# Kernel optimization log

Measured on AMD Instinct MI355X. Metric: run time of the kernel, lower is better.

Reference implementation:

```python
import jax, jax.numpy as jnp
import numpy as np

B, S, D, H = 2, 2048, 2048, 16
DK = D // H


def setup_inputs() -> dict:
    key = jax.random.key(0)
    k1, k2, k3 = jax.random.split(key, 3)
    x = jax.random.normal(k1, (B, S, D), dtype=jnp.float32)
    # trunc-normal in the original; plain normal with matching std is fine for a numeric baseline
    std_qkv = 2.0 / (DK + D)  # note: original passes variance as std to trunc_normal_
    W_qkv = jax.random.normal(k2, (3 * D, D), dtype=jnp.float32) * std_qkv
    W_o = jax.random.normal(k3, (D, D), dtype=jnp.float32) * (1.0 / D)
    return {"x": x, "W_qkv": W_qkv, "W_o": W_o}


def reference(x, W_qkv, W_o):
    b, s, d = x.shape
    # fused QKV projection: y = x @ W_qkv^T
    qkv = jnp.einsum('bsd,ed->bse', x, W_qkv)  # [b, s, 3d]
    q, k, v = jnp.split(qkv, 3, axis=-1)
    # [b, s, d] -> [b, h, s, dk]
    def to_heads(t):
        return t.reshape(b, s, H, DK).transpose(0, 2, 1, 3)
    q, k, v = to_heads(q), to_heads(k), to_heads(v)
    scores = jnp.einsum('bhqd,bhkd->bhqk', q, k) / np.sqrt(DK).astype(np.float32)
    causal = jnp.tril(jnp.ones((s, s), dtype=bool))
    scores = jnp.where(causal, scores, -jnp.inf)
    att = jax.nn.softmax(scores, axis=-1)
    out = jnp.einsum('bhqk,bhkd->bhqd', att, v)  # [b, h, s, dk]
    out = out.transpose(0, 2, 1, 3).reshape(b, s, d)
    return jnp.einsum('bsd,od->bso', out, W_o)
```

## Files before the change

kernel.cpp:

```cpp
#include <hip/hip_runtime.h>

typedef _Float16 f16;
typedef _Float16 f16x4 __attribute__((ext_vector_type(4)));
typedef _Float16 f16x8 __attribute__((ext_vector_type(8)));
typedef float    f32x4 __attribute__((ext_vector_type(4)));

#define MFMA_F16(a,b,c) __builtin_amdgcn_mfma_f32_16x16x32_f16((a),(b),(c),0,0,0)

static constexpr int B_  = 2;
static constexpr int S_  = 2048;
static constexpr int D_  = 2048;
static constexpr int H_  = 16;
static constexpr int DK_ = 128;
static constexpr int K_  = 2048;

__device__ __forceinline__ void gload_lds16(const void* g, void* l) {
  __builtin_amdgcn_global_load_lds(
      (const __attribute__((address_space(1))) void*)g,
      (__attribute__((address_space(3))) void*)l, 16, 0, 0);
}

__global__ __launch_bounds__(256) void cast_all_kernel(const float* __restrict__ x,
                                                       const float* __restrict__ wqkv,
                                                       const float* __restrict__ wo,
                                                       f16* __restrict__ xb,
                                                       f16* __restrict__ wqkvb,
                                                       f16* __restrict__ wob) {
  const int total = 6291456;
  int i = blockIdx.x * 256 + threadIdx.x;
  int stride = gridDim.x * 256;
  for (int j = i; j < total; j += stride) {
    const float* src; f16* dst; int jj;
    if (j < 2097152)      { src = x;    dst = xb;    jj = j; }
    else if (j < 5242880) { src = wqkv; dst = wqkvb; jj = j - 2097152; }
    else                  { src = wo;   dst = wob;   jj = j - 5242880; }
    float4 v = reinterpret_cast<const float4*>(src)[jj];
    f16x4 o = {(f16)v.x, (f16)v.y, (f16)v.z, (f16)v.w};
    reinterpret_cast<f16x4*>(dst)[jj] = o;
  }
}


#define SYNCW0                                          \
  asm volatile("s_waitcnt vmcnt(0)" ::: "memory");      \
  __builtin_amdgcn_s_barrier();                         \
  asm volatile("" ::: "memory");

__device__ __forceinline__ void stage2(const f16* gA, const f16* gB, char* slot, int w) {
  gload_lds16(gA,      slot +         w * 1024);
  gload_lds16(gA + 32, slot +  8192 + w * 1024);
  gload_lds16(gB,      slot + 16384 + w * 1024);
  gload_lds16(gB + 32, slot + 24576 + w * 1024);
}

__device__ __forceinline__ void compute2(const char* slot, int aoff, int boff, int lro,
                                         f32x4 (&acc)[4][2]) {
  f16x8 a0[4], b0[2], a1[4], b1[2];
#pragma unroll
  for (int mi = 0; mi < 4; ++mi) {
    a0[mi] = *(const f16x8*)(slot +        aoff + mi * 1024 + lro);
    a1[mi] = *(const f16x8*)(slot + 8192 + aoff + mi * 1024 + lro);
  }
#pragma unroll
  for (int ni = 0; ni < 2; ++ni) {
    b0[ni] = *(const f16x8*)(slot + 16384 + boff + ni * 1024 + lro);
    b1[ni] = *(const f16x8*)(slot + 24576 + boff + ni * 1024 + lro);
  }
  __builtin_amdgcn_s_setprio(1);
#pragma unroll
  for (int mi = 0; mi < 4; ++mi)
#pragma unroll
    for (int ni = 0; ni < 2; ++ni)
      acc[mi][ni] = MFMA_F16(a0[mi], b0[ni], acc[mi][ni]);
#pragma unroll
  for (int mi = 0; mi < 4; ++mi)
#pragma unroll
    for (int ni = 0; ni < 2; ++ni)
      acc[mi][ni] = MFMA_F16(a1[mi], b1[ni], acc[mi][ni]);
  __builtin_amdgcn_s_setprio(0);
}

__device__ __forceinline__ void gemm_core_db(const f16* __restrict__ A,
                                             const f16* __restrict__ Bw,
                                             int brow, int bcol, char* lds,
                                             f32x4 (&acc)[4][2]) {
  const int tid = threadIdx.x;
  const int w = tid >> 6, l = tid & 63;
  const int lg = l >> 4, lr = l & 15;
  const int wm = w >> 2, wn = w & 3;
  const int lro = (lr * 4 + (lg ^ ((lr >> 1) & 3))) * 16;
  const int aoff = wm * 4096;
  const int boff = wn * 2048;

#pragma unroll
  for (int mi = 0; mi < 4; ++mi)
#pragma unroll
    for (int ni = 0; ni < 2; ++ni) acc[mi][ni] = (f32x4){0.f, 0.f, 0.f, 0.f};

  const int kgsrc = (l & 3) ^ ((l >> 3) & 3);
  const f16* gA = A  + (size_t)(brow * 128 + w * 16 + (l >> 2)) * K_ + kgsrc * 8;
  const f16* gB = Bw + (size_t)(bcol * 128 + w * 16 + (l >> 2)) * K_ + kgsrc * 8;

  char* s0 = lds;
  char* s1 = lds + 32768;

  stage2(gA, gB, s0, w);
  SYNCW0

  for (int tb = 0; tb < 16; ++tb) {
    const int t = tb * 2;
    stage2(gA + (size_t)(t + 1) * 64, gB + (size_t)(t + 1) * 64, s1, w);
    compute2(s0, aoff, boff, lro, acc);
    SYNCW0
    if (tb < 15)
      stage2(gA + (size_t)(t + 2) * 64, gB + (size_t)(t + 2) * 64, s0, w);
    compute2(s1, aoff, boff, lro, acc);
    SYNCW0
  }
}

__global__ __launch_bounds__(512, 4) void gemm_qkv_kernel(const f16* __restrict__ xb,
                                                          const f16* __restrict__ wqkv,
                                                          f16* __restrict__ Q,
                                                          f16* __restrict__ Kk,
                                                          f16* __restrict__ Vt) {
  __shared__ __align__(16) char lds[65536];
  const int bid = blockIdx.x;
  const int xcd = bid & 7;
  const int local = bid >> 3;
  const int brow = xcd * 4 + (local & 3);
  const int bcol = local >> 2;

  f32x4 acc[4][2];
  gemm_core_db(xb, wqkv, brow, bcol, lds, acc);

  const int tid = threadIdx.x;
  const int w = tid >> 6, l = tid & 63;
  const int lg = l >> 4, lr = l & 15;
  const int wm = w >> 2, wn = w & 3;

  const int which = bcol >> 4;
  const int h = bcol & 15;

  if (which == 2) {
#pragma unroll
    for (int mi = 0; mi < 4; ++mi) {
      const int m0 = brow * 128 + wm * 64 + mi * 16 + lg * 4;
      const int b = m0 >> 11, s = m0 & 2047;
#pragma unroll
      for (int ni = 0; ni < 2; ++ni) {
        const int dk = wn * 32 + ni * 16 + lr;
        f16x4 v = {(f16)acc[mi][ni][0], (f16)acc[mi][ni][1],
                   (f16)acc[mi][ni][2], (f16)acc[mi][ni][3]};
        *(f16x4*)(Vt + ((size_t)(b * H_ + h) * DK_ + dk) * S_ + s) = v;
      }
    }
  } else {
    f16* outp = (which == 0) ? Q : Kk;
    const float scale = (which == 0) ? 0.08838834764831845f : 1.0f;
#pragma unroll
    for (int mi = 0; mi < 4; ++mi) {
      const int m0 = brow * 128 + wm * 64 + mi * 16 + lg * 4;
#pragma unroll
      for (int ni = 0; ni < 2; ++ni) {
        const int dk = wn * 32 + ni * 16 + lr;
#pragma unroll
        for (int r = 0; r < 4; ++r) {
          const int mm = m0 + r;
          const int b = mm >> 11, s = mm & 2047;
          outp[(((size_t)b * H_ + h) * S_ + s) * DK_ + dk] = (f16)(acc[mi][ni][r] * scale);
        }
      }
    }
  }
}

__global__ __launch_bounds__(512, 4) void gemm_out_kernel(const f16* __restrict__ ab,
                                                          const f16* __restrict__ wo,
                                                          float* __restrict__ out) {
  __shared__ __align__(16) char lds[65536];
  const int bid = blockIdx.x;
  const int xcd = bid & 7;
  const int local = bid >> 3;
  const int brow = xcd * 4 + (local & 3);
  const int bcol = local >> 2;

  f32x4 acc[4][2];
  gemm_core_db(ab, wo, brow, bcol, lds, acc);

  const int tid = threadIdx.x;
  const int w = tid >> 6, l = tid & 63;
  const int lg = l >> 4, lr = l & 15;
  const int wm = w >> 2, wn = w & 3;

#pragma unroll
  for (int mi = 0; mi < 4; ++mi) {
    const int m0 = brow * 128 + wm * 64 + mi * 16 + lg * 4;
#pragma unroll
    for (int ni = 0; ni < 2; ++ni) {
      const int n = bcol * 128 + wn * 32 + ni * 16 + lr;
#pragma unroll
      for (int r = 0; r < 4; ++r)
        out[(size_t)(m0 + r) * D_ + n] = acc[mi][ni][r];
    }
  }
}

__global__ __launch_bounds__(256) void attn_kernel(const f16* __restrict__ Q,
                                                   const f16* __restrict__ Kg,
                                                   const f16* __restrict__ Vt,
                                                   f16* __restrict__ O) {
  __shared__ __align__(16) char Kbuf2[2][16384];
  __shared__ __align__(16) char Vbuf2[2][16384];
  __shared__ __align__(16) unsigned char Ps[4][2048];

  const int bid = blockIdx.x;
  const int pr = bid & 15;
  const int h  = (bid >> 4) & 15;
  const int b  = bid >> 8;
  const int bh = b * H_ + h;
  const int tid = threadIdx.x;
  const int w = tid >> 6, l = tid & 63;
  const int lg = l >> 4, lr = l & 15;
  const int lrow = l >> 2;
  const int kgsrc = (l & 3) ^ ((l >> 3) & 3);
  const int lro = (lr * 4 + (lg ^ ((lr >> 1) & 3))) * 16;

  const f16* Kbase = Kg + (size_t)bh * S_ * DK_;
  const f16* Vbase = Vt + (size_t)bh * DK_ * S_;

  for (int half = 0; half < 2; ++half) {
    const int qt = half ? (31 - pr) : pr;

    const f16* Qg = Q + ((size_t)bh * S_ + qt * 64 + w * 16) * DK_;
    f16x8 qf[4];
#pragma unroll
    for (int kd = 0; kd < 4; ++kd)
      qf[kd] = *(const f16x8*)(Qg + (size_t)lr * DK_ + kd * 32 + lg * 8);

    f32x4 o[8];
#pragma unroll
    for (int n = 0; n < 8; ++n) o[n] = (f32x4){0.f, 0.f, 0.f, 0.f};
    float mrun[4] = {-1e30f, -1e30f, -1e30f, -1e30f};
    float lrun[4] = {0.f, 0.f, 0.f, 0.f};

    const int ntiles = qt + 1;

    {
      const f16* Kt = Kbase;
      const f16* Vp = Vbase;
#pragma unroll
      for (int i = 0; i < 4; ++i) {
        const int u = w * 4 + i;
        gload_lds16(Kt + (size_t)((u >> 2) * 16 + lrow) * DK_ + (u & 3) * 32 + kgsrc * 8,
                    Kbuf2[0] + u * 1024);
      }
#pragma unroll
      for (int i = 0; i < 4; ++i) {
        const int u = w * 4 + i;
        gload_lds16(Vp + (size_t)((u >> 1) * 16 + lrow) * S_ + (u & 1) * 32 + kgsrc * 8,
                    Vbuf2[0] + u * 1024);
      }
    }

    for (int kt = 0; kt < ntiles; ++kt) {
      const int cur = kt & 1;
      if (kt + 1 < ntiles) {
        const f16* Kt = Kbase + (size_t)(kt + 1) * 64 * DK_;
        const f16* Vp = Vbase + (kt + 1) * 64;
        char* Kb = Kbuf2[cur ^ 1];
        char* Vb = Vbuf2[cur ^ 1];
#pragma unroll
        for (int i = 0; i < 4; ++i) {
          const int u = w * 4 + i;
          gload_lds16(Kt + (size_t)((u >> 2) * 16 + lrow) * DK_ + (u & 3) * 32 + kgsrc * 8,
                      Kb + u * 1024);
        }
#pragma unroll
        for (int i = 0; i < 4; ++i) {
          const int u = w * 4 + i;
          gload_lds16(Vp + (size_t)((u >> 1) * 16 + lrow) * S_ + (u & 1) * 32 + kgsrc * 8,
                      Vb + u * 1024);
        }
        asm volatile("s_waitcnt vmcnt(8)" ::: "memory");
      } else {
        asm volatile("s_waitcnt vmcnt(0)" ::: "memory");
      }
      __builtin_amdgcn_s_barrier();

      const char* Kb = Kbuf2[cur];
      const char* Vb = Vbuf2[cur];

      f32x4 s[4];
#pragma unroll
      for (int j = 0; j < 4; ++j) s[j] = (f32x4){0.f, 0.f, 0.f, 0.f};
      __builtin_amdgcn_s_setprio(1);
#pragma unroll
      for (int j = 0; j < 4; ++j) {
#pragma unroll
        for (int kd = 0; kd < 4; ++kd) {
          f16x8 kf = *(const f16x8*)(Kb + ((j << 2) + kd) * 1024 + lro);
          s[j] = MFMA_F16(qf[kd], kf, s[j]);
        }
      }
      __builtin_amdgcn_s_setprio(0);
      if (kt == qt) {
#pragma unroll
        for (int j = 0; j < 4; ++j) {
          const int col = j * 16 + lr;
#pragma unroll
          for (int r = 0; r < 4; ++r) {
            const int qrow = w * 16 + lg * 4 + r;
            if (col > qrow) s[j][r] = -1e30f;
          }
        }
      }
      float scl[4];
#pragma unroll
      for (int r = 0; r < 4; ++r) {
        float m0 = fmaxf(fmaxf(s[0][r], s[1][r]), fmaxf(s[2][r], s[3][r]));
#pragma unroll
        for (int msk = 1; msk < 16; msk <<= 1) m0 = fmaxf(m0, __shfl_xor(m0, msk, 64));
        const float nm = fmaxf(mrun[r], m0);
        scl[r] = __expf(mrun[r] - nm);
        mrun[r] = nm;
      }
      float rs[4] = {0.f, 0.f, 0.f, 0.f};
#pragma unroll
      for (int j = 0; j < 4; ++j) {
#pragma unroll
        for (int r = 0; r < 4; ++r) {
          const float p = __expf(fmaxf(s[j][r] - mrun[r], -80.f));
          rs[r] += p;
          const int row = lg * 4 + r;
          const int cb = (j * 16 + lr) * 2;
          *(f16*)(Ps[w] + row * 128 + (cb ^ ((row & 7) << 4))) = (f16)p;
        }
      }
#pragma unroll
      for (int r = 0; r < 4; ++r) {
        float t = rs[r];
#pragma unroll
        for (int msk = 1; msk < 16; msk <<= 1) t += __shfl_xor(t, msk, 64);
        lrun[r] = lrun[r] * scl[r] + t;
      }
#pragma unroll
      for (int n = 0; n < 8; ++n)
#pragma unroll
        for (int r = 0; r < 4; ++r) o[n][r] *= scl[r];

      asm volatile("s_waitcnt lgkmcnt(0)" ::: "memory");

      __builtin_amdgcn_s_setprio(1);
#pragma unroll
      for (int ks = 0; ks < 2; ++ks) {
        f16x8 pf = *(const f16x8*)(Ps[w] + lr * 128 + ((ks * 64 + lg * 16) ^ ((lr & 7) << 4)));
#pragma unroll
        for (int n = 0; n < 8; ++n) {
          f16x8 vf = *(const f16x8*)(Vb + ((n << 1) + ks) * 1024 + lro);
          o[n] = MFMA_F16(pf, vf, o[n]);
        }
      }
      __builtin_amdgcn_s_setprio(0);
      __builtin_amdgcn_s_barrier();
    }

#pragma unroll
    for (int r = 0; r < 4; ++r) {
      const float inv = 1.0f / lrun[r];
      const int srow = qt * 64 + w * 16 + lg * 4 + r;
      f16* op = O + ((size_t)b * S_ + srow) * D_ + h * DK_;
#pragma unroll
      for (int n = 0; n < 8; ++n) op[n * 16 + lr] = (f16)(o[n][r] * inv);
    }
  }
}

extern "C" void kernel_launch(void* const* d_in, const int* in_sizes, int n_in,
                              void* d_out, int out_size, void* d_ws, size_t ws_size,
                              hipStream_t stream) {
  const float* x    = (const float*)d_in[0];
  const float* wqkv = (const float*)d_in[1];
  const float* wo   = (const float*)d_in[2];
  float* out = (float*)d_out;
  char* ws = (char*)d_ws;

  f16* xb     = (f16*)(ws + 0);
  f16* wqkvb  = (f16*)(ws + 16777216);
  f16* wob    = (f16*)(ws + 41943040);
  f16* Qb     = (f16*)(ws + 50331648);
  f16* Kb     = (f16*)(ws + 67108864);
  f16* Vtb    = (f16*)(ws + 83886080);
  f16* attn_o = (f16*)(ws + 0);

  cast_all_kernel<<<2048, 256, 0, stream>>>(x, wqkv, wo, xb, wqkvb, wob);

  gemm_qkv_kernel<<<1536, 512, 0, stream>>>(xb, wqkvb, Qb, Kb, Vtb);
  attn_kernel<<<512, 256, 0, stream>>>(Qb, Kb, Vtb, attn_o);
  gemm_out_kernel<<<512, 512, 0, stream>>>(attn_o, wob, out);
}
```

Baseline: 266.9 us.

## Process 128 query rows per attention block to reuse K/V tiles

The attention kernel now assigns 128 query rows per block (32 per wave, two 16-row MFMA subtiles) instead of 64, so each K/V tile loaded into LDS serves twice as many query rows. Waves skip compute on tiles past their own causal boundary while still joining the barriers. The grid halves to 256 blocks, and the accumulator and Q-fragment register arrays double. The intent is to cut K/V load traffic and barrier overhead per unit of work, at the cost of fewer blocks and higher register pressure.

```diff
diff --git a/kernel.cpp b/kernel.cpp
--- a/kernel.cpp
+++ b/kernel.cpp
@@ -212,12 +212,12 @@
                                                    f16* __restrict__ O) {
   __shared__ __align__(16) char Kbuf2[2][16384];
   __shared__ __align__(16) char Vbuf2[2][16384];
-  __shared__ __align__(16) unsigned char Ps[4][2048];
+  __shared__ __align__(16) unsigned char Ps[4][4096];
 
   const int bid = blockIdx.x;
-  const int pr = bid & 15;
-  const int h  = (bid >> 4) & 15;
-  const int b  = bid >> 8;
+  const int pr = bid & 7;
+  const int h  = (bid >> 3) & 15;
+  const int b  = bid >> 7;
   const int bh = b * H_ + h;
   const int tid = threadIdx.x;
   const int w = tid >> 6, l = tid & 63;
@@ -230,37 +230,40 @@
   const f16* Vbase = Vt + (size_t)bh * DK_ * S_;
 
   for (int half = 0; half < 2; ++half) {
-    const int qt = half ? (31 - pr) : pr;
-
-    const f16* Qg = Q + ((size_t)bh * S_ + qt * 64 + w * 16) * DK_;
-    f16x8 qf[4];
-#pragma unroll
-    for (int kd = 0; kd < 4; ++kd)
-      qf[kd] = *(const f16x8*)(Qg + (size_t)lr * DK_ + kd * 32 + lg * 8);
-
-    f32x4 o[8];
-#pragma unroll
-    for (int n = 0; n < 8; ++n) o[n] = (f32x4){0.f, 0.f, 0.f, 0.f};
-    float mrun[4] = {-1e30f, -1e30f, -1e30f, -1e30f};
-    float lrun[4] = {0.f, 0.f, 0.f, 0.f};
-
-    const int ntiles = qt + 1;
-
-    {
-      const f16* Kt = Kbase;
-      const f16* Vp = Vbase;
-#pragma unroll
-      for (int i = 0; i < 4; ++i) {
-        const int u = w * 4 + i;
-        gload_lds16(Kt + (size_t)((u >> 2) * 16 + lrow) * DK_ + (u & 3) * 32 + kgsrc * 8,
-                    Kbuf2[0] + u * 1024);
-      }
-#pragma unroll
-      for (int i = 0; i < 4; ++i) {
-        const int u = w * 4 + i;
-        gload_lds16(Vp + (size_t)((u >> 1) * 16 + lrow) * S_ + (u & 1) * 32 + kgsrc * 8,
-                    Vbuf2[0] + u * 1024);
-      }
+    const int qt = half ? (15 - pr) : pr;
+    const int lastkt = 2 * qt + (w >> 1);
+    const int ntiles = 2 * qt + 2;
+
+    const f16* Qg = Q + ((size_t)bh * S_ + qt * 128 + w * 32) * DK_;
+    f16x8 qf[2][4];
+#pragma unroll
+    for (int mi = 0; mi < 2; ++mi)
+#pragma unroll
+      for (int kd = 0; kd < 4; ++kd)
+        qf[mi][kd] = *(const f16x8*)(Qg + (size_t)(mi * 16 + lr) * DK_ + kd * 32 + lg * 8);
+
+    f32x4 o[2][8];
+#pragma unroll
+    for (int mi = 0; mi < 2; ++mi)
+#pragma unroll
+      for (int n = 0; n < 8; ++n) o[mi][n] = (f32x4){0.f, 0.f, 0.f, 0.f};
+    float mrun[2][4], lrun[2][4];
+#pragma unroll
+    for (int mi = 0; mi < 2; ++mi)
+#pragma unroll
+      for (int r = 0; r < 4; ++r) { mrun[mi][r] = -1e30f; lrun[mi][r] = 0.f; }
+
+#pragma unroll
+    for (int i = 0; i < 4; ++i) {
+      const int u = w * 4 + i;
+      gload_lds16(Kbase + (size_t)((u >> 2) * 16 + lrow) * DK_ + (u & 3) * 32 + kgsrc * 8,
+                  Kbuf2[0] + u * 1024);
+    }
+#pragma unroll
+    for (int i = 0; i < 4; ++i) {
+      const int u = w * 4 + i;
+      gload_lds16(Vbase + (size_t)((u >> 1) * 16 + lrow) * S_ + (u & 1) * 32 + kgsrc * 8,
+                  Vbuf2[0] + u * 1024);
     }
 
     for (int kt = 0; kt < ntiles; ++kt) {
@@ -288,91 +291,107 @@
       }
       __builtin_amdgcn_s_barrier();
 
-      const char* Kb = Kbuf2[cur];
-      const char* Vb = Vbuf2[cur];
-
-      f32x4 s[4];
-#pragma unroll
-      for (int j = 0; j < 4; ++j) s[j] = (f32x4){0.f, 0.f, 0.f, 0.f};
-      __builtin_amdgcn_s_setprio(1);
-#pragma unroll
-      for (int j = 0; j < 4; ++j) {
-#pragma unroll
-        for (int kd = 0; kd < 4; ++kd) {
-          f16x8 kf = *(const f16x8*)(Kb + ((j << 2) + kd) * 1024 + lro);
-          s[j] = MFMA_F16(qf[kd], kf, s[j]);
-        }
+      if (kt <= lastkt) {
+        const char* Kb = Kbuf2[cur];
+        const char* Vb = Vbuf2[cur];
+
+        f32x4 s[2][4];
+#pragma unroll
+        for (int mi = 0; mi < 2; ++mi)
+#pragma unroll
+          for (int j = 0; j < 4; ++j) s[mi][j] = (f32x4){0.f, 0.f, 0.f, 0.f};
+        __builtin_amdgcn_s_setprio(1);
+#pragma unroll
+        for (int j = 0; j < 4; ++j) {
+#pragma unroll
+          for (int kd = 0; kd < 4; ++kd) {
+            f16x8 kf = *(const f16x8*)(Kb + ((j << 2) + kd) * 1024 + lro);
+            s[0][j] = MFMA_F16(qf[0][kd], kf, s[0][j]);
+            s[1][j] = MFMA_F16(qf[1][kd], kf, s[1][j]);
+          }
+        }
+        __builtin_amdgcn_s_setprio(0);
+        if (kt == lastkt) {
+#pragma unroll
+          for (int mi = 0; mi < 2; ++mi)
+#pragma unroll
+            for (int j = 0; j < 4; ++j) {
+              const int col = kt * 64 + j * 16 + lr;
+#pragma unroll
+              for (int r = 0; r < 4; ++r) {
+                const int qrow = qt * 128 + w * 32 + mi * 16 + lg * 4 + r;
+                if (col > qrow) s[mi][j][r] = -1e30f;
+              }
+            }
+        }
+#pragma unroll
+        for (int mi = 0; mi < 2; ++mi) {
+          float scl[4];
+#pragma unroll
+          for (int r = 0; r < 4; ++r) {
+            float m0 = fmaxf(fmaxf(s[mi][0][r], s[mi][1][r]), fmaxf(s[mi][2][r], s[mi][3][r]));
+#pragma unroll
+            for (int msk = 1; msk < 16; msk <<= 1) m0 = fmaxf(m0, __shfl_xor(m0, msk, 64));
+            const float nm = fmaxf(mrun[mi][r], m0);
+            scl[r] = __expf(mrun[mi][r] - nm);
+            mrun[mi][r] = nm;
+          }
+          float rs[4] = {0.f, 0.f, 0.f, 0.f};
+#pragma unroll
+          for (int j = 0; j < 4; ++j) {
+#pragma unroll
+            for (int r = 0; r < 4; ++r) {
+              const float p = __expf(fmaxf(s[mi][j][r] - mrun[mi][r], -80.f));
+              rs[r] += p;
+              const int row = mi * 16 + lg * 4 + r;
+              const int cb = (j * 16 + lr) * 2;
+              *(f16*)(Ps[w] + row * 128 + (cb ^ ((row & 7) << 4))) = (f16)p;
+            }
+          }
+#pragma unroll
+          for (int r = 0; r < 4; ++r) {
+            float t = rs[r];
+#pragma unroll
+            for (int msk = 1; msk < 16; msk <<= 1) t += __shfl_xor(t, msk, 64);
+            lrun[mi][r] = lrun[mi][r] * scl[r] + t;
+          }
+#pragma unroll
+          for (int n = 0; n < 8; ++n)
+#pragma unroll
+            for (int r = 0; r < 4; ++r) o[mi][n][r] *= scl[r];
+        }
+
+        asm volatile("s_waitcnt lgkmcnt(0)" ::: "memory");
+
+        __builtin_amdgcn_s_setprio(1);
+#pragma unroll
+        for (int ks = 0; ks < 2; ++ks) {
+          f16x8 pf0 = *(const f16x8*)(Ps[w] + (lr) * 128 +
+                                      ((ks * 64 + lg * 16) ^ ((lr & 7) << 4)));
+          f16x8 pf1 = *(const f16x8*)(Ps[w] + (16 + lr) * 128 +
+                                      ((ks * 64 + lg * 16) ^ ((lr & 7) << 4)));
+#pragma unroll
+          for (int n = 0; n < 8; ++n) {
+            f16x8 vf = *(const f16x8*)(Vb + ((n << 1) + ks) * 1024 + lro);
+            o[0][n] = MFMA_F16(pf0, vf, o[0][n]);
+            o[1][n] = MFMA_F16(pf1, vf, o[1][n]);
+          }
+        }
+        __builtin_amdgcn_s_setprio(0);
       }
-      __builtin_amdgcn_s_setprio(0);
-      if (kt == qt) {
-#pragma unroll
-        for (int j = 0; j < 4; ++j) {
-          const int col = j * 16 + lr;
-#pragma unroll
-          for (int r = 0; r < 4; ++r) {
-            const int qrow = w * 16 + lg * 4 + r;
-            if (col > qrow) s[j][r] = -1e30f;
-          }
-        }
+      __builtin_amdgcn_s_barrier();
+    }
+
+#pragma unroll
+    for (int mi = 0; mi < 2; ++mi)
+#pragma unroll
+      for (int r = 0; r < 4; ++r) {
+        const float inv = 1.0f / lrun[mi][r];
+        const int srow = qt * 128 + w * 32 + mi * 16 + lg * 4 + r;
+        f16* op = O + ((size_t)b * S_ + srow) * D_ + h * DK_;
+#pragma unroll
+        for (int n = 0; n < 8; ++n) op[n * 16 + lr] = (f16)(o[mi][n][r] * inv);
       }
-      float scl[4];
-#pragma unroll
-      for (int r = 0; r < 4; ++r) {
-        float m0 = fmaxf(fmaxf(s[0][r], s[1][r]), fmaxf(s[2][r], s[3][r]));
-#pragma unroll
-        for (int msk = 1; msk < 16; msk <<= 1) m0 = fmaxf(m0, __shfl_xor(m0, msk, 64));
-        const float nm = fmaxf(mrun[r], m0);
-        scl[r] = __expf(mrun[r] - nm);
-        mrun[r] = nm;
-      }
-      float rs[4] = {0.f, 0.f, 0.f, 0.f};
-#pragma unroll
-      for (int j = 0; j < 4; ++j) {
-#pragma unroll
-        for (int r = 0; r < 4; ++r) {
-          const float p = __expf(fmaxf(s[j][r] - mrun[r], -80.f));
-          rs[r] += p;
-          const int row = lg * 4 + r;
-          const int cb = (j * 16 + lr) * 2;
-          *(f16*)(Ps[w] + row * 128 + (cb ^ ((row & 7) << 4))) = (f16)p;
-        }
-      }
-#pragma unroll
-      for (int r = 0; r < 4; ++r) {
-        float t = rs[r];
-#pragma unroll
-        for (int msk = 1; msk < 16; msk <<= 1) t += __shfl_xor(t, msk, 64);
-        lrun[r] = lrun[r] * scl[r] + t;
-      }
-#pragma unroll
-      for (int n = 0; n < 8; ++n)
-#pragma unroll
-        for (int r = 0; r < 4; ++r) o[n][r] *= scl[r];
-
-      asm volatile("s_waitcnt lgkmcnt(0)" ::: "memory");
-
-      __builtin_amdgcn_s_setprio(1);
-#pragma unroll
-      for (int ks = 0; ks < 2; ++ks) {
-        f16x8 pf = *(const f16x8*)(Ps[w] + lr * 128 + ((ks * 64 + lg * 16) ^ ((lr & 7) << 4)));
-#pragma unroll
-        for (int n = 0; n < 8; ++n) {
-          f16x8 vf = *(const f16x8*)(Vb + ((n << 1) + ks) * 1024 + lro);
-          o[n] = MFMA_F16(pf, vf, o[n]);
-        }
-      }
-      __builtin_amdgcn_s_setprio(0);
-      __builtin_amdgcn_s_barrier();
-    }
-
-#pragma unroll
-    for (int r = 0; r < 4; ++r) {
-      const float inv = 1.0f / lrun[r];
-      const int srow = qt * 64 + w * 16 + lg * 4 + r;
-      f16* op = O + ((size_t)b * S_ + srow) * D_ + h * DK_;
-#pragma unroll
-      for (int n = 0; n < 8; ++n) op[n * 16 + lr] = (f16)(o[n][r] * inv);
-    }
   }
 }
 
@@ -396,6 +415,6 @@
   cast_all_kernel<<<2048, 256, 0, stream>>>(x, wqkv, wo, xb, wqkvb, wob);
 
   gemm_qkv_kernel<<<1536, 512, 0, stream>>>(xb, wqkvb, Qb, Kb, Vtb);
-  attn_kernel<<<512, 256, 0, stream>>>(Qb, Kb, Vtb, attn_o);
+  attn_kernel<<<256, 256, 0, stream>>>(Qb, Kb, Vtb, attn_o);
   gemm_out_kernel<<<512, 512, 0, stream>>>(attn_o, wob, out);
 }
```

Result: slower. 321.4 us (+20.4%).
